# Optimization experiments

Measured on AMD Instinct MI355X. Metric: run time of the kernel, lower is better.

The kernel has to match this reference:

```python
import math
import jax, jax.numpy as jnp
import numpy as np

B, S, IN, D, H, F, E, K, L, C = 4, 1024, 768, 512, 8, 2048, 8, 2, 2, 2
DH = D // H
TEMP = 1.0
LBW = 0.01
EPS = 1e-5


def _sinusoidal_pe(seq_len, dim):
    pos = jnp.arange(seq_len, dtype=jnp.float32)[:, None]
    div = jnp.exp(jnp.arange(0, dim, 2, dtype=jnp.float32) * (-math.log(10000.0) / dim))
    sin = jnp.sin(pos * div)  # [S, D/2]
    cos = jnp.cos(pos * div)  # [S, D/2]
    return jnp.stack([sin, cos], axis=-1).reshape(seq_len, dim)  # interleave even=sin, odd=cos


def _layernorm(x, scale, bias):
    mu = jnp.mean(x, axis=-1, keepdims=True)
    var = jnp.var(x, axis=-1, keepdims=True)
    return (x - mu) * jax.lax.rsqrt(var + EPS) * scale + bias


def _attention(x, w, b):
    # w: [4, D, D] (q, k, v, out), b: [4, D]
    bsz, slen, _ = x.shape
    q = (x @ w[0] + b[0]).reshape(bsz, slen, H, DH)
    k = (x @ w[1] + b[1]).reshape(bsz, slen, H, DH)
    v = (x @ w[2] + b[2]).reshape(bsz, slen, H, DH)
    scores = jnp.einsum('bqhd,bkhd->bhqk', q, k) / math.sqrt(DH)
    attn = jax.nn.softmax(scores, axis=-1)
    out = jnp.einsum('bhqk,bkhd->bqhd', attn, v).reshape(bsz, slen, D)
    return out @ w[3] + b[3]


def _moe(x_flat, gate_w, gate_b, w1, b1, w2, b2):
    # x_flat: [T, D]; gate_w: [D, E]; w1: [E, D, F]; w2: [E, F, D]
    T = x_flat.shape[0]
    gate_logits = (x_flat @ gate_w + gate_b) / TEMP
    gate_scores = jax.nn.softmax(gate_logits, axis=-1)  # [T, E]
    top_v, top_i = jax.lax.top_k(gate_scores, K)        # [T, K]
    top_v = top_v / jnp.sum(top_v, axis=-1, keepdims=True)
    # combine weight per (token, expert): sum over k of topv * one_hot(topi)
    oh = jax.nn.one_hot(top_i, E, dtype=x_flat.dtype)   # [T, K, E]
    combine = jnp.einsum('tk,tke->te', top_v, oh)       # [T, E]
    # dense per-expert FFN (reference for the masked gather/scatter loop)
    h = jax.nn.gelu(jnp.einsum('td,edf->etf', x_flat, w1) + b1[:, None, :], approximate=False)
    expert_out = jnp.einsum('etf,efd->etd', h, w2) + b2[:, None, :]  # [E, T, D]
    y = jnp.einsum('te,etd->td', combine, expert_out)
    # load-balance auxiliary loss
    counts = jnp.sum(oh, axis=(0, 1))                   # [E]
    frac = counts / (T * K)
    routing = jnp.mean(gate_scores, axis=0)
    aux = E * jnp.sum(frac * routing)
    return y, aux


def setup_inputs() -> dict:
    key = jax.random.key(0)
    ks = jax.random.split(key, 10)
    rn = lambda k, shape: jax.random.normal(k, shape, jnp.float32) * 0.02
    return {
        'x': jax.random.normal(ks[0], (B, S, IN), jnp.float32),
        'proj_w': rn(ks[1], (IN, D)), 'proj_b': jnp.zeros((D,), jnp.float32),
        'attn_w': rn(ks[2], (L, 4, D, D)), 'attn_b': jnp.zeros((L, 4, D), jnp.float32),
        'ln1_s': jnp.ones((L, D), jnp.float32), 'ln1_b': jnp.zeros((L, D), jnp.float32),
        'gate_w': rn(ks[3], (L, D, E)), 'gate_b': jnp.zeros((L, E), jnp.float32),
        'w1': rn(ks[4], (L, E, D, F)), 'b1': jnp.zeros((L, E, F), jnp.float32),
        'w2': rn(ks[5], (L, E, F, D)), 'b2': jnp.zeros((L, E, D), jnp.float32),
        'ln2_s': jnp.ones((L, D), jnp.float32), 'ln2_b': jnp.zeros((L, D), jnp.float32),
        'cls_w': rn(ks[6], (D, C)), 'cls_b': jnp.zeros((C,), jnp.float32),
    }


def reference(x, proj_w, proj_b, attn_w, attn_b, ln1_s, ln1_b, gate_w, gate_b,
              w1, b1, w2, b2, ln2_s, ln2_b, cls_w, cls_b):
    h = x @ proj_w + proj_b                       # [B, S, D]
    h = h + _sinusoidal_pe(S, D)[None, :, :]
    total_aux = jnp.zeros((), h.dtype)
    for l in range(L):
        attn_out = _attention(h, attn_w[l], attn_b[l])
        h = _layernorm(h + attn_out, ln1_s[l], ln1_b[l])
        ffn_out, aux = _moe(h.reshape(-1, D), gate_w[l], gate_b[l],
                            w1[l], b1[l], w2[l], b2[l])
        total_aux = total_aux + aux
        h = _layernorm(h + ffn_out.reshape(B, S, D), ln2_s[l], ln2_b[l])
    pooled = jnp.mean(h, axis=1)                  # [B, D]
    logits = pooled @ cls_w + cls_b               # [B, C]
    return logits, LBW * total_aux
```

## Files before the change

kernel.cpp:

```cpp
#include <hip/hip_runtime.h>
#include <math.h>

#define B_ 4
#define S_ 1024
#define IN_ 768
#define D_ 512
#define H_ 8
#define F_ 2048
#define E_ 8
#define KTOP_ 2
#define L_ 2
#define C_ 2
#define DH_ 64
#define T_ (B_*S_)
#define EPS_ 1e-5f
#define LBW_ 0.01f
#define QLD_ (3*D_)
#define NBG_ (T_/256)
#define PSPL_ 16

typedef unsigned short u16;
typedef __attribute__((ext_vector_type(8))) unsigned short u16x8;
typedef __attribute__((ext_vector_type(4))) unsigned short u16x4;
typedef __attribute__((ext_vector_type(8))) short short8;
typedef __attribute__((ext_vector_type(4))) float f32x4;

__device__ __forceinline__ u16 f2b(float f) {
  union { float f; unsigned u; } v; v.f = f;
  const unsigned u = v.u;
  return (u16)((u + 0x7FFFu + ((u >> 16) & 1u)) >> 16);
}
__device__ __forceinline__ float b2f(u16 s) {
  union { unsigned u; float f; } v; v.u = ((unsigned)s) << 16;
  return v.f;
}

__device__ __forceinline__ void gl2lds16(const u16* g, u16* l) {
  __builtin_amdgcn_global_load_lds(
      (const __attribute__((address_space(1))) unsigned int*)g,
      (__attribute__((address_space(3))) unsigned int*)l, 16, 0, 0);
}

__global__ __launch_bounds__(256) void castT(
    const float* __restrict__ W, u16* __restrict__ WT, int K, int N)
{
  __shared__ float tile[32][33];
  const size_t mo = (size_t)blockIdx.z * K * N;
  const int n0 = blockIdx.x * 32, k0 = blockIdx.y * 32;
  const int t = threadIdx.x;
  const int kr = t >> 3, nc4 = (t & 7) * 4;
  const float4 v = *(const float4*)(W + mo + (size_t)(k0 + kr) * N + n0 + nc4);
  tile[kr][nc4+0] = v.x; tile[kr][nc4+1] = v.y;
  tile[kr][nc4+2] = v.z; tile[kr][nc4+3] = v.w;
  __syncthreads();
  const int nr = t >> 3, kc4 = (t & 7) * 4;
  u16x4 o;
  #pragma unroll
  for (int i = 0; i < 4; ++i) o[i] = f2b(tile[kc4 + i][nr]);
  *(u16x4*)(WT + mo + (size_t)(n0 + nr) * K + k0 + kc4) = o;
}

__global__ __launch_bounds__(256) void cast_x(
    const float* __restrict__ X, u16* __restrict__ Xb)
{
  const size_t i = ((size_t)blockIdx.x * 256 + threadIdx.x) * 8;
  const float4 a = *(const float4*)(X + i);
  const float4 b = *(const float4*)(X + i + 4);
  u16x8 o;
  o[0]=f2b(a.x); o[1]=f2b(a.y); o[2]=f2b(a.z); o[3]=f2b(a.w);
  o[4]=f2b(b.x); o[5]=f2b(b.y); o[6]=f2b(b.z); o[7]=f2b(b.w);
  *(u16x8*)(Xb + i) = o;
}

template<int BN, int PE, int GELU, int WF32, int WBF16, int GATHER, int MOE>
__global__ __launch_bounds__(256) void gemm_gl(
    const u16* __restrict__ A, const u16* __restrict__ WTb,
    const float* __restrict__ biasb, float* __restrict__ Cf,
    u16* __restrict__ Cb, int N, int K,
    const int* __restrict__ idx_list, const int* __restrict__ offsets,
    const int* __restrict__ counts)
{
  constexpr int BM = 128;
  constexpr int MI = 4;
  constexpr int MJ = BN / 32;
  constexpr int NIB = BN / 32;
  __shared__ __align__(16) u16 Atile[BM][64];
  __shared__ __align__(16) u16 Btile[BN][64];
  __shared__ int rowsrc[MOE ? BM : 1];

  const int tid = threadIdx.x;
  const int row0 = blockIdx.y * BM, col0 = blockIdx.x * BN;

  int cnt = 0, off = 0;
  const u16* WT = WTb;
  const float* bias = biasb;
  if constexpr (MOE) {
    const int e = blockIdx.z;
    cnt = counts[e];
    if (row0 >= cnt) return;
    off = offsets[e];
    WT  = WTb + (size_t)e * K * N;
    bias = biasb + (size_t)e * N;
    if (tid < BM) {
      const int rr = row0 + tid;
      rowsrc[tid] = (rr < cnt) ? (GATHER ? idx_list[off + rr] : (off + rr)) : 0;
    }
    __syncthreads();
  }

  const int w = tid >> 6, lane = tid & 63;
  const int q15 = lane & 15, g = lane >> 4;
  const int lrow8 = lane >> 3;
  const int scol = ((lane & 7) ^ lrow8) * 8;

  const u16* aptr[4];
  #pragma unroll
  for (int t = 0; t < 4; ++t) {
    const int arow = w * 32 + t * 8 + lrow8;
    int grow;
    if constexpr (MOE) grow = rowsrc[arow];
    else               grow = row0 + arow;
    aptr[t] = A + (size_t)grow * K + scol;
  }
  const u16* bptr[NIB];
  #pragma unroll
  for (int t = 0; t < NIB; ++t) {
    const int brow = w * (BN / 4) + t * 8 + lrow8;
    bptr[t] = WT + (size_t)(col0 + brow) * K + scol;
  }

  const int ar0 = (w >> 1) * 64;
  const int bc0 = (w & 1) * (BN / 2);

  f32x4 acc[MI][MJ];
  #pragma unroll
  for (int i = 0; i < MI; ++i)
    #pragma unroll
    for (int j = 0; j < MJ; ++j) acc[i][j] = (f32x4){0.f, 0.f, 0.f, 0.f};

  for (int k0 = 0; k0 < K; k0 += 64) {
    #pragma unroll
    for (int t = 0; t < 4; ++t)
      gl2lds16(aptr[t] + k0, &Atile[w * 32 + t * 8][0]);
    #pragma unroll
    for (int t = 0; t < NIB; ++t)
      gl2lds16(bptr[t] + k0, &Btile[w * (BN / 4) + t * 8][0]);
    asm volatile("s_waitcnt vmcnt(0)" ::: "memory");
    __syncthreads();
    #pragma unroll
    for (int c = 0; c < 2; ++c) {
      const int ps = ((c * 4 + g) ^ (q15 & 7)) * 8;
      short8 af[MI], bfv[MJ];
      #pragma unroll
      for (int i = 0; i < MI; ++i)
        af[i] = *(const short8*)&Atile[ar0 + i * 16 + q15][ps];
      #pragma unroll
      for (int j = 0; j < MJ; ++j)
        bfv[j] = *(const short8*)&Btile[bc0 + j * 16 + q15][ps];
      #pragma unroll
      for (int i = 0; i < MI; ++i)
        #pragma unroll
        for (int j = 0; j < MJ; ++j)
          acc[i][j] = __builtin_amdgcn_mfma_f32_16x16x32_bf16(af[i], bfv[j], acc[i][j], 0, 0, 0);
    }
    __syncthreads();
  }

  #pragma unroll
  for (int i = 0; i < MI; ++i) {
    #pragma unroll
    for (int r = 0; r < 4; ++r) {
      const int lrow = ar0 + i * 16 + g * 4 + r;
      if constexpr (MOE) {
        const int rr = row0 + lrow;
        if (rr >= cnt) continue;
        const size_t gidx = (size_t)off + rr;
        #pragma unroll
        for (int j = 0; j < MJ; ++j) {
          const int c = col0 + bc0 + j * 16 + q15;
          float vv = acc[i][j][r] + bias[c];
          if (GELU) vv = 0.5f * vv * (1.0f + erff(vv * 0.7071067811865475f));
          if (WF32) Cf[gidx * N + c] = vv;
          if (WBF16) Cb[gidx * N + c] = f2b(vv);
        }
      } else {
        const int row = row0 + lrow;
        #pragma unroll
        for (int j = 0; j < MJ; ++j) {
          const int c = col0 + bc0 + j * 16 + q15;
          float vv = acc[i][j][r] + bias[c];
          if (PE) {
            const float kfac = -0.03597789207803197f;
            const float div = expf((float)(c >> 1) * kfac);
            const float ang = (float)(row & (S_ - 1)) * div;
            vv += (c & 1) ? cosf(ang) : sinf(ang);
          }
          if (WF32) Cf[(size_t)row * N + c] = vv;
          if (WBF16) Cb[(size_t)row * N + c] = f2b(vv);
        }
      }
    }
  }
}

__global__ __launch_bounds__(256) void attn_mfma(
    const u16* __restrict__ qkv, u16* __restrict__ og)
{
  __shared__ u16 Kl[32][72];
  __shared__ u16 VTl[64 * 34];
  const int qt = blockIdx.x;
  const int hh = blockIdx.y & 7, b = blockIdx.y >> 3;
  const int tid = threadIdx.x;
  const int w = tid >> 6, lane = tid & 63;
  const int g = lane >> 4, q15 = lane & 15;
  const int skv = tid >> 3, sd8 = (tid & 7) * 8;

  const size_t qrow = (size_t)(b * S_ + qt * 64 + w * 16 + q15) * QLD_ + hh * 64;
  const short8 qf0 = *(const short8*)(qkv + qrow + g * 8);
  const short8 qf1 = *(const short8*)(qkv + qrow + 32 + g * 8);

  f32x4 o0 = {0.f,0.f,0.f,0.f}, o1 = {0.f,0.f,0.f,0.f};
  f32x4 o2 = {0.f,0.f,0.f,0.f}, o3 = {0.f,0.f,0.f,0.f};
  float m = -1e30f, l = 0.f;

  for (int c0 = 0; c0 < S_; c0 += 32) {
    const size_t srow = (size_t)(b * S_ + c0 + skv) * QLD_ + hh * 64 + sd8;
    const u16x8 kv8 = *(const u16x8*)(qkv + srow + D_);
    const u16x8 vv8 = *(const u16x8*)(qkv + srow + 2 * D_);
    *(u16x8*)&Kl[skv][sd8] = kv8;
    #pragma unroll
    for (int j = 0; j < 8; ++j) {
      const int d = sd8 + j;
      const int kvp = skv ^ (((d >> 5) & 1) << 3);
      VTl[d * 34 + kvp] = vv8[j];
    }
    __syncthreads();

    f32x4 st0 = {0.f,0.f,0.f,0.f}, st1 = {0.f,0.f,0.f,0.f};
    {
      const short8 kf00 = *(const short8*)&Kl[q15][g * 8];
      const short8 kf01 = *(const short8*)&Kl[q15][32 + g * 8];
      const short8 kf10 = *(const short8*)&Kl[16 + q15][g * 8];
      const short8 kf11 = *(const short8*)&Kl[16 + q15][32 + g * 8];
      st0 = __builtin_amdgcn_mfma_f32_16x16x32_bf16(kf00, qf0, st0, 0, 0, 0);
      st0 = __builtin_amdgcn_mfma_f32_16x16x32_bf16(kf01, qf1, st0, 0, 0, 0);
      st1 = __builtin_amdgcn_mfma_f32_16x16x32_bf16(kf10, qf0, st1, 0, 0, 0);
      st1 = __builtin_amdgcn_mfma_f32_16x16x32_bf16(kf11, qf1, st1, 0, 0, 0);
    }

    float s0[4], s1[4];
    #pragma unroll
    for (int r = 0; r < 4; ++r) { s0[r] = st0[r] * 0.125f; s1[r] = st1[r] * 0.125f; }
    float cm = s0[0];
    #pragma unroll
    for (int r = 1; r < 4; ++r) cm = fmaxf(cm, s0[r]);
    #pragma unroll
    for (int r = 0; r < 4; ++r) cm = fmaxf(cm, s1[r]);
    cm = fmaxf(cm, __shfl_xor(cm, 16));
    cm = fmaxf(cm, __shfl_xor(cm, 32));
    const float mn = fmaxf(m, cm);
    const float rsc = __expf(m - mn);
    m = mn;
    float p0[4], p1[4];
    float rs = 0.f;
    #pragma unroll
    for (int r = 0; r < 4; ++r) { p0[r] = __expf(s0[r] - mn); rs += p0[r]; }
    #pragma unroll
    for (int r = 0; r < 4; ++r) { p1[r] = __expf(s1[r] - mn); rs += p1[r]; }
    rs += __shfl_xor(rs, 16);
    rs += __shfl_xor(rs, 32);
    l = l * rsc + rs;

    float rq[4];
    #pragma unroll
    for (int r = 0; r < 4; ++r) rq[r] = __shfl(rsc, 4 * g + r);
    #pragma unroll
    for (int r = 0; r < 4; ++r) {
      o0[r] *= rq[r]; o1[r] *= rq[r]; o2[r] *= rq[r]; o3[r] *= rq[r];
    }

    unsigned pk[4];
    #pragma unroll
    for (int r = 0; r < 4; ++r)
      asm("v_cvt_pk_bf16_f32 %0, %1, %2" : "=v"(pk[r]) : "v"(p0[r]), "v"(p1[r]));
    u16x8 pf;
    #pragma unroll
    for (int j = 0; j < 8; ++j) {
      const int src = q15 + 16 * ((j >> 2) + 2 * (g & 1));
      const unsigned pv = (unsigned)__shfl((int)pk[j & 3], src);
      pf[j] = (g >= 2) ? (u16)(pv >> 16) : (u16)(pv & 0xffffu);
    }
    const short8 pfs = *(const short8*)&pf;

    #pragma unroll
    for (int dt = 0; dt < 4; ++dt) {
      const int gsw = g ^ (dt >> 1);
      const u16* vp = &VTl[(dt * 16 + q15) * 34 + 8 * gsw];
      union { unsigned u[4]; short8 s8; } yv;
      yv.u[0] = *(const unsigned*)(vp + 0);
      yv.u[1] = *(const unsigned*)(vp + 2);
      yv.u[2] = *(const unsigned*)(vp + 4);
      yv.u[3] = *(const unsigned*)(vp + 6);
      if (dt == 0) o0 = __builtin_amdgcn_mfma_f32_16x16x32_bf16(pfs, yv.s8, o0, 0, 0, 0);
      if (dt == 1) o1 = __builtin_amdgcn_mfma_f32_16x16x32_bf16(pfs, yv.s8, o1, 0, 0, 0);
      if (dt == 2) o2 = __builtin_amdgcn_mfma_f32_16x16x32_bf16(pfs, yv.s8, o2, 0, 0, 0);
      if (dt == 3) o3 = __builtin_amdgcn_mfma_f32_16x16x32_bf16(pfs, yv.s8, o3, 0, 0, 0);
    }
    __syncthreads();
  }

  const float linv = 1.0f / l;
  float lq[4];
  #pragma unroll
  for (int r = 0; r < 4; ++r) lq[r] = __shfl(linv, 4 * g + r);
  #pragma unroll
  for (int r = 0; r < 4; ++r) {
    const size_t tok = (size_t)(b * S_ + qt * 64 + w * 16 + 4 * g + r);
    u16* orow = og + tok * D_ + hh * 64 + q15;
    orow[0]  = f2b(o0[r] * lq[r]);
    orow[16] = f2b(o1[r] * lq[r]);
    orow[32] = f2b(o2[r] * lq[r]);
    orow[48] = f2b(o3[r] * lq[r]);
  }
}

__device__ __forceinline__ void load8(const float* p, float* a) {
  const float4 v0 = *(const float4*)p;
  const float4 v1 = *(const float4*)(p + 4);
  a[0]=v0.x; a[1]=v0.y; a[2]=v0.z; a[3]=v0.w;
  a[4]=v1.x; a[5]=v1.y; a[6]=v1.z; a[7]=v1.w;
}

template<int MODE>
__global__ __launch_bounds__(64) void ln_kernel(
    float* __restrict__ h, u16* __restrict__ hb,
    const float* __restrict__ add,
    const float* __restrict__ ebuf, const int* __restrict__ pos_tk,
    const float* __restrict__ topw,
    const float* __restrict__ sc, const float* __restrict__ bi)
{
  const int t = blockIdx.x;
  const int lane = threadIdx.x;
  const int d0 = lane * 8;
  float* hrow = h + (size_t)t * D_;
  float x[8];
  load8(hrow + d0, x);
  if (MODE == 0) {
    float a[8]; load8(add + (size_t)t * D_ + d0, a);
    #pragma unroll
    for (int i = 0; i < 8; ++i) x[i] += a[i];
  } else {
    const float w0 = topw[2*t], w1 = topw[2*t+1];
    const int p0 = pos_tk[2*t], p1 = pos_tk[2*t+1];
    float a[8], b[8];
    load8(ebuf + (size_t)p0 * D_ + d0, a);
    load8(ebuf + (size_t)p1 * D_ + d0, b);
    #pragma unroll
    for (int i = 0; i < 8; ++i) x[i] += w0 * a[i] + w1 * b[i];
  }
  float s = 0.f, ss = 0.f;
  #pragma unroll
  for (int i = 0; i < 8; ++i) { s += x[i]; ss += x[i] * x[i]; }
  #pragma unroll
  for (int off = 32; off > 0; off >>= 1) {
    s  += __shfl_xor(s,  off);
    ss += __shfl_xor(ss, off);
  }
  const float mu = s * (1.f / D_);
  const float var = ss * (1.f / D_) - mu * mu;
  const float rstd = rsqrtf(var + EPS_);
  float g[8], be[8];
  load8(sc + d0, g); load8(bi + d0, be);
  float y[8];
  #pragma unroll
  for (int i = 0; i < 8; ++i) y[i] = (x[i] - mu) * rstd * g[i] + be[i];
  float4 oo0, oo1;
  oo0.x=y[0]; oo0.y=y[1]; oo0.z=y[2]; oo0.w=y[3];
  oo1.x=y[4]; oo1.y=y[5]; oo1.z=y[6]; oo1.w=y[7];
  *(float4*)(hrow + d0) = oo0;
  *(float4*)(hrow + d0 + 4) = oo1;
  u16x8 ob;
  #pragma unroll
  for (int i = 0; i < 8; ++i) ob[i] = f2b(y[i]);
  *(u16x8*)(hb + (size_t)t * D_ + d0) = ob;
}

__global__ __launch_bounds__(256) void gate_kernel(
    const float* __restrict__ h, const float* __restrict__ gw,
    const float* __restrict__ gb,
    int* __restrict__ top_i, float* __restrict__ top_w,
    int* __restrict__ counts_p, float* __restrict__ routing_p)
{
  __shared__ float s_rout[E_];
  __shared__ int s_cnt[E_];
  const int tid = threadIdx.x;
  if (tid < E_) { s_rout[tid] = 0.f; s_cnt[tid] = 0; }
  __syncthreads();
  const int t = blockIdx.x * 256 + tid;
  const float* xr = h + (size_t)t * D_;
  float logit[E_] = {};
  for (int d = 0; d < D_; d += 4) {
    const float4 xv = *(const float4*)(xr + d);
    const float xs[4] = {xv.x, xv.y, xv.z, xv.w};
    #pragma unroll
    for (int i = 0; i < 4; ++i)
      #pragma unroll
      for (int e = 0; e < E_; ++e)
        logit[e] = fmaf(xs[i], gw[(size_t)(d+i) * E_ + e], logit[e]);
  }
  float mx = -1e30f;
  #pragma unroll
  for (int e = 0; e < E_; ++e) { logit[e] += gb[e]; mx = fmaxf(mx, logit[e]); }
  float p[E_]; float sum = 0.f;
  #pragma unroll
  for (int e = 0; e < E_; ++e) { p[e] = expf(logit[e] - mx); sum += p[e]; }
  const float inv = 1.0f / sum;
  #pragma unroll
  for (int e = 0; e < E_; ++e) p[e] *= inv;
  int i0 = 0; float v0 = p[0];
  #pragma unroll
  for (int e = 1; e < E_; ++e) if (p[e] > v0) { v0 = p[e]; i0 = e; }
  int i1 = -1; float v1 = -1.f;
  #pragma unroll
  for (int e = 0; e < E_; ++e) if (e != i0 && p[e] > v1) { v1 = p[e]; i1 = e; }
  const float sw = 1.0f / (v0 + v1);
  top_i[2*t] = i0; top_i[2*t+1] = i1;
  top_w[2*t] = v0 * sw; top_w[2*t+1] = v1 * sw;
  atomicAdd(&s_cnt[i0], 1); atomicAdd(&s_cnt[i1], 1);
  #pragma unroll
  for (int e = 0; e < E_; ++e) atomicAdd(&s_rout[e], p[e]);
  __syncthreads();
  if (tid < E_) {
    counts_p[blockIdx.x * E_ + tid] = s_cnt[tid];
    routing_p[blockIdx.x * E_ + tid] = s_rout[tid];
  }
}

__global__ void gate_scan(
    const int* __restrict__ counts_p, const float* __restrict__ routing_p,
    int* __restrict__ counts, int* __restrict__ offsets,
    int* __restrict__ blk_base, float* __restrict__ aux_acc, int first)
{
  if (threadIdx.x == 0) {
    int cnt[E_]; float rout[E_];
    for (int e = 0; e < E_; ++e) { cnt[e] = 0; rout[e] = 0.f; }
    for (int b = 0; b < NBG_; ++b)
      for (int e = 0; e < E_; ++e) {
        cnt[e] += counts_p[b * E_ + e];
        rout[e] += routing_p[b * E_ + e];
      }
    int off = 0; float aux = 0.f;
    int run[E_];
    for (int e = 0; e < E_; ++e) {
      counts[e] = cnt[e];
      offsets[e] = off; run[e] = off; off += cnt[e];
      aux += ((float)cnt[e] / (float)(T_ * KTOP_)) * (rout[e] / (float)T_);
    }
    for (int b = 0; b < NBG_; ++b)
      for (int e = 0; e < E_; ++e) {
        blk_base[b * E_ + e] = run[e];
        run[e] += counts_p[b * E_ + e];
      }
    const float v = (float)E_ * aux;
    *aux_acc = first ? v : (*aux_acc + v);
  }
}

__global__ __launch_bounds__(256) void gate_fill(
    const int* __restrict__ top_i, const int* __restrict__ blk_base,
    int* __restrict__ idx_list, int* __restrict__ pos_tk)
{
  __shared__ int s_cur[E_];
  const int tid = threadIdx.x;
  if (tid < E_) s_cur[tid] = 0;
  __syncthreads();
  const int t = blockIdx.x * 256 + tid;
  const int e0 = top_i[2*t], e1 = top_i[2*t+1];
  const int r0 = atomicAdd(&s_cur[e0], 1);
  const int r1 = atomicAdd(&s_cur[e1], 1);
  const int g0 = blk_base[blockIdx.x * E_ + e0] + r0;
  const int g1 = blk_base[blockIdx.x * E_ + e1] + r1;
  idx_list[g0] = t; pos_tk[2*t]   = g0;
  idx_list[g1] = t; pos_tk[2*t+1] = g1;
}

__global__ __launch_bounds__(256) void pool_part(
    const float* __restrict__ h, float* __restrict__ ppart)
{
  const int b = blockIdx.y, d0 = blockIdx.x * 64, z = blockIdx.z;
  const int tid = threadIdx.x;
  const int dl = tid & 63, sg = tid >> 6;
  const int s0 = z * (S_ / PSPL_);
  float s = 0.f;
  #pragma unroll
  for (int si = sg; si < S_ / PSPL_; si += 4)
    s += h[((size_t)b * S_ + s0 + si) * D_ + d0 + dl];
  __shared__ float part[4][64];
  part[sg][dl] = s;
  __syncthreads();
  if (tid < 64) {
    const float v = part[0][tid] + part[1][tid] + part[2][tid] + part[3][tid];
    ppart[((size_t)z * B_ + b) * D_ + d0 + tid] = v;
  }
}

__global__ __launch_bounds__(256) void pool_reduce(
    const float* __restrict__ ppart, float* __restrict__ pooled)
{
  const int idx = blockIdx.x * 256 + threadIdx.x;
  float s = 0.f;
  #pragma unroll
  for (int z = 0; z < PSPL_; ++z)
    s += ppart[(size_t)z * B_ * D_ + idx];
  pooled[idx] = s * (1.0f / S_);
}

__global__ __launch_bounds__(64) void cls_kernel(
    const float* __restrict__ pooled, const float* __restrict__ cls_w,
    const float* __restrict__ cls_b, const float* __restrict__ aux_acc,
    float* __restrict__ out)
{
  const int t = threadIdx.x;
  if (t < B_ * C_) {
    const int b = t >> 1, c = t & 1;
    float acc = cls_b[c];
    for (int d = 0; d < D_; ++d)
      acc = fmaf(pooled[b * D_ + d], cls_w[(size_t)d * C_ + c], acc);
    out[b * C_ + c] = acc;
  }
  if (t == 32) out[B_ * C_] = LBW_ * (*aux_acc);
}

extern "C" void kernel_launch(void* const* d_in, const int* in_sizes, int n_in,
                              void* d_out, int out_size, void* d_ws, size_t ws_size,
                              hipStream_t stream) {
  const float* x      = (const float*)d_in[0];
  const float* proj_w = (const float*)d_in[1];
  const float* proj_b = (const float*)d_in[2];
  const float* attn_w = (const float*)d_in[3];
  const float* attn_b = (const float*)d_in[4];
  const float* ln1_s  = (const float*)d_in[5];
  const float* ln1_b  = (const float*)d_in[6];
  const float* gate_w = (const float*)d_in[7];
  const float* gate_b = (const float*)d_in[8];
  const float* w1     = (const float*)d_in[9];
  const float* b1     = (const float*)d_in[10];
  const float* w2     = (const float*)d_in[11];
  const float* b2     = (const float*)d_in[12];
  const float* ln2_s  = (const float*)d_in[13];
  const float* ln2_b  = (const float*)d_in[14];
  const float* cls_w  = (const float*)d_in[15];
  const float* cls_b  = (const float*)d_in[16];
  float* out = (float*)d_out;

  char* base = (char*)d_ws;
  float* h      = (float*)base;                 base += (size_t)T_ * D_ * 4;
  float* t2     = (float*)base;                 base += (size_t)T_ * D_ * 4;
  float* ebuf   = (float*)base;                 base += (size_t)T_ * KTOP_ * D_ * 4;
  u16*   qkvb   = (u16*)base;                   base += (size_t)T_ * QLD_ * 2;
  u16*   x_bf   = (u16*)base;                   base += (size_t)T_ * IN_ * 2;
  u16*   h_bf   = (u16*)base;                   base += (size_t)T_ * D_ * 2;
  u16*   t1_bf  = (u16*)base;                   base += (size_t)T_ * D_ * 2;
  char*  big    = base;                         base += (size_t)T_ * KTOP_ * F_ * 2;
  u16*   wscr   = (u16*)base;                   base += (size_t)E_ * D_ * F_ * 2;
  float* topw   = (float*)base;                 base += (size_t)T_ * KTOP_ * 4;
  int*   counts_p = (int*)base;                 base += NBG_ * E_ * 4;
  float* routing_p= (float*)base;               base += NBG_ * E_ * 4;
  int*   blk_base = (int*)base;                 base += NBG_ * E_ * 4;
  int*   counts = (int*)base;                   base += E_ * 4;
  float* aux_acc= (float*)base;                 base += 4;
  int*   offsets= (int*)base;                   base += E_ * 4;
  int*   top_i  = (int*)base;                   base += (size_t)T_ * KTOP_ * 4;
  int*   idx_list=(int*)base;                   base += (size_t)T_ * KTOP_ * 4;
  int*   pos_tk = (int*)base;                   base += (size_t)T_ * KTOP_ * 4;
  float* pooled = (float*)base;                 base += (size_t)B_ * D_ * 4;
  float* ppart  = (float*)base;                 base += (size_t)PSPL_ * B_ * D_ * 4;

  u16* hbuf_bf = (u16*)big;

  cast_x<<<(T_ * IN_) / 2048, 256, 0, stream>>>(x, x_bf);
  castT<<<dim3(D_/32, IN_/32, 1), 256, 0, stream>>>(proj_w, wscr, IN_, D_);
  gemm_gl<64, 1, 0, 1, 1, 0, 0><<<dim3(D_/64, T_/128), 256, 0, stream>>>(
      x_bf, wscr, proj_b, h, h_bf, D_, IN_, nullptr, nullptr, nullptr);

  for (int l = 0; l < L_; ++l) {
    castT<<<dim3(D_/32, D_/32, 4), 256, 0, stream>>>(
        attn_w + (size_t)l*4*D_*D_, wscr, D_, D_);

    gemm_gl<128, 0, 0, 0, 1, 0, 0><<<dim3(QLD_/128, T_/128), 256, 0, stream>>>(
        h_bf, wscr, attn_b + (size_t)l*4*D_, nullptr, qkvb, QLD_, D_,
        nullptr, nullptr, nullptr);
    attn_mfma<<<dim3(S_/64, B_*H_), 256, 0, stream>>>(qkvb, t1_bf);
    gemm_gl<64, 0, 0, 1, 0, 0, 0><<<dim3(D_/64, T_/128), 256, 0, stream>>>(
        t1_bf, wscr + (size_t)3*D_*D_, attn_b + (size_t)(l*4+3)*D_, t2, nullptr,
        D_, D_, nullptr, nullptr, nullptr);
    ln_kernel<0><<<T_, 64, 0, stream>>>(h, h_bf, t2, nullptr, nullptr, nullptr,
                                        ln1_s + (size_t)l*D_, ln1_b + (size_t)l*D_);

    gate_kernel<<<NBG_, 256, 0, stream>>>(h, gate_w + (size_t)l*D_*E_,
                                          gate_b + (size_t)l*E_,
                                          top_i, topw, counts_p, routing_p);
    gate_scan<<<1, 64, 0, stream>>>(counts_p, routing_p, counts, offsets,
                                    blk_base, aux_acc, l == 0 ? 1 : 0);
    gate_fill<<<NBG_, 256, 0, stream>>>(top_i, blk_base, idx_list, pos_tk);

    castT<<<dim3(F_/32, D_/32, E_), 256, 0, stream>>>(
        w1 + (size_t)l*E_*D_*F_, wscr, D_, F_);
    gemm_gl<128, 0, 1, 0, 1, 1, 1><<<dim3(F_/128, (T_*KTOP_)/128, E_), 256, 0, stream>>>(
        h_bf, wscr, b1 + (size_t)l*E_*F_, nullptr, hbuf_bf,
        F_, D_, idx_list, offsets, counts);
    castT<<<dim3(D_/32, F_/32, E_), 256, 0, stream>>>(
        w2 + (size_t)l*E_*F_*D_, wscr, F_, D_);
    gemm_gl<128, 0, 0, 1, 0, 0, 1><<<dim3(D_/128, (T_*KTOP_)/128, E_), 256, 0, stream>>>(
        hbuf_bf, wscr, b2 + (size_t)l*E_*D_, ebuf, nullptr,
        D_, F_, idx_list, offsets, counts);
    ln_kernel<1><<<T_, 64, 0, stream>>>(h, h_bf, nullptr, ebuf, pos_tk, topw,
                                        ln2_s + (size_t)l*D_, ln2_b + (size_t)l*D_);
  }

  pool_part<<<dim3(D_/64, B_, PSPL_), 256, 0, stream>>>(h, ppart);
  pool_reduce<<<(B_*D_)/256, 256, 0, stream>>>(ppart, pooled);
  cls_kernel<<<1, 64, 0, stream>>>(pooled, cls_w, cls_b, aux_acc, out);
}
```

Measured before the change: 573.7 us.

## Double-buffer LDS tiles in GEMM to overlap global loads with MFMA

Turns the single-stage GEMM main loop into a two-stage LDS ping-pong. The next K-tile is loaded while the current one is consumed, with partial vmcnt waits and raw s_barrier calls. It also raises wave priority with s_setprio around the MFMA section. The goal is to hide global-to-LDS latency, at the cost of doubling LDS use, which may lower occupancy, and of relying on exact vmcnt counts per BN.

```diff
diff --git a/kernel.cpp b/kernel.cpp
--- a/kernel.cpp
+++ b/kernel.cpp
@@ -84,8 +84,8 @@
   constexpr int MI = 4;
   constexpr int MJ = BN / 32;
   constexpr int NIB = BN / 32;
-  __shared__ __align__(16) u16 Atile[BM][64];
-  __shared__ __align__(16) u16 Btile[BN][64];
+  __shared__ __align__(16) u16 Atile[2][BM][64];
+  __shared__ __align__(16) u16 Btile[2][BN][64];
   __shared__ int rowsrc[MOE ? BM : 1];
 
   const int tid = threadIdx.x;
@@ -138,32 +138,48 @@
     #pragma unroll
     for (int j = 0; j < MJ; ++j) acc[i][j] = (f32x4){0.f, 0.f, 0.f, 0.f};
 
-  for (int k0 = 0; k0 < K; k0 += 64) {
+  auto STAGE = [&](int buf, int k0) {
     #pragma unroll
     for (int t = 0; t < 4; ++t)
-      gl2lds16(aptr[t] + k0, &Atile[w * 32 + t * 8][0]);
+      gl2lds16(aptr[t] + k0, &Atile[buf][w * 32 + t * 8][0]);
     #pragma unroll
     for (int t = 0; t < NIB; ++t)
-      gl2lds16(bptr[t] + k0, &Btile[w * (BN / 4) + t * 8][0]);
-    asm volatile("s_waitcnt vmcnt(0)" ::: "memory");
-    __syncthreads();
+      gl2lds16(bptr[t] + k0, &Btile[buf][w * (BN / 4) + t * 8][0]);
+  };
+
+  STAGE(0, 0);
+  const int NT = K >> 6;
+  for (int t = 0; t < NT; ++t) {
+    const int cur = t & 1;
+    if (t + 1 < NT) {
+      STAGE(cur ^ 1, (t + 1) << 6);
+      if constexpr (BN == 128)
+        asm volatile("s_waitcnt vmcnt(8)" ::: "memory");
+      else
+        asm volatile("s_waitcnt vmcnt(6)" ::: "memory");
+    } else {
+      asm volatile("s_waitcnt vmcnt(0)" ::: "memory");
+    }
+    __builtin_amdgcn_s_barrier();
+    __builtin_amdgcn_s_setprio(1);
     #pragma unroll
     for (int c = 0; c < 2; ++c) {
       const int ps = ((c * 4 + g) ^ (q15 & 7)) * 8;
       short8 af[MI], bfv[MJ];
       #pragma unroll
       for (int i = 0; i < MI; ++i)
-        af[i] = *(const short8*)&Atile[ar0 + i * 16 + q15][ps];
+        af[i] = *(const short8*)&Atile[cur][ar0 + i * 16 + q15][ps];
       #pragma unroll
       for (int j = 0; j < MJ; ++j)
-        bfv[j] = *(const short8*)&Btile[bc0 + j * 16 + q15][ps];
+        bfv[j] = *(const short8*)&Btile[cur][bc0 + j * 16 + q15][ps];
       #pragma unroll
       for (int i = 0; i < MI; ++i)
         #pragma unroll
         for (int j = 0; j < MJ; ++j)
           acc[i][j] = __builtin_amdgcn_mfma_f32_16x16x32_bf16(af[i], bfv[j], acc[i][j], 0, 0, 0);
     }
-    __syncthreads();
+    __builtin_amdgcn_s_setprio(0);
+    __builtin_amdgcn_s_barrier();
   }
 
   #pragma unroll
```

New measurement: 583.7 us. Within noise of the previous version (+1.7%).

## Split K across two blocks for out-projection and MoE down GEMMs

Applied to the files above, without the earlier changes.

Adds a KSPLIT template parameter so the attention out-projection and the MoE second GEMM launch twice as many blocks, each covering half the K range. Each half writes its partial sums to a separate slab of doubled fp32 buffers, and the following layernorm kernels add the two partials. The aim is more blocks in flight on these low-occupancy GEMMs. The cost is extra fp32 partial writes and reads in the layernorm kernels, plus a larger workspace.

```diff
diff --git a/kernel.cpp b/kernel.cpp
--- a/kernel.cpp
+++ b/kernel.cpp
@@ -72,7 +72,8 @@
   *(u16x8*)(Xb + i) = o;
 }
 
-template<int BN, int PE, int GELU, int WF32, int WBF16, int GATHER, int MOE>
+template<int BN, int PE, int GELU, int WF32, int WBF16, int GATHER, int MOE,
+         int KSPLIT>
 __global__ __launch_bounds__(256) void gemm_gl(
     const u16* __restrict__ A, const u16* __restrict__ WTb,
     const float* __restrict__ biasb, float* __restrict__ Cf,
@@ -84,6 +85,7 @@
   constexpr int MI = 4;
   constexpr int MJ = BN / 32;
   constexpr int NIB = BN / 32;
+  constexpr int SROWS = MOE ? (T_ * KTOP_) : T_;
   __shared__ __align__(16) u16 Atile[BM][64];
   __shared__ __align__(16) u16 Btile[BN][64];
   __shared__ int rowsrc[MOE ? BM : 1];
@@ -91,11 +93,14 @@
   const int tid = threadIdx.x;
   const int row0 = blockIdx.y * BM, col0 = blockIdx.x * BN;
 
+  int ks = 0;
   int cnt = 0, off = 0;
   const u16* WT = WTb;
   const float* bias = biasb;
   if constexpr (MOE) {
-    const int e = blockIdx.z;
+    int e;
+    if constexpr (KSPLIT == 2) { e = blockIdx.z >> 1; ks = blockIdx.z & 1; }
+    else                       { e = blockIdx.z; }
     cnt = counts[e];
     if (row0 >= cnt) return;
     off = offsets[e];
@@ -106,7 +111,11 @@
       rowsrc[tid] = (rr < cnt) ? (GATHER ? idx_list[off + rr] : (off + rr)) : 0;
     }
     __syncthreads();
-  }
+  } else {
+    if constexpr (KSPLIT == 2) ks = blockIdx.z;
+  }
+  const int k_beg = ks * (K / KSPLIT);
+  const int k_end = k_beg + (K / KSPLIT);
 
   const int w = tid >> 6, lane = tid & 63;
   const int q15 = lane & 15, g = lane >> 4;
@@ -138,7 +147,7 @@
     #pragma unroll
     for (int j = 0; j < MJ; ++j) acc[i][j] = (f32x4){0.f, 0.f, 0.f, 0.f};
 
-  for (int k0 = 0; k0 < K; k0 += 64) {
+  for (int k0 = k_beg; k0 < k_end; k0 += 64) {
     #pragma unroll
     for (int t = 0; t < 4; ++t)
       gl2lds16(aptr[t] + k0, &Atile[w * 32 + t * 8][0]);
@@ -166,6 +175,7 @@
     __syncthreads();
   }
 
+  const size_t srow_off = (size_t)ks * SROWS;
   #pragma unroll
   for (int i = 0; i < MI; ++i) {
     #pragma unroll
@@ -174,29 +184,33 @@
       if constexpr (MOE) {
         const int rr = row0 + lrow;
         if (rr >= cnt) continue;
-        const size_t gidx = (size_t)off + rr;
+        const size_t gidx = (size_t)off + rr + srow_off;
         #pragma unroll
         for (int j = 0; j < MJ; ++j) {
           const int c = col0 + bc0 + j * 16 + q15;
-          float vv = acc[i][j][r] + bias[c];
+          float bv = bias[c];
+          if (KSPLIT == 2 && ks == 1) bv = 0.f;
+          float vv = acc[i][j][r] + bv;
           if (GELU) vv = 0.5f * vv * (1.0f + erff(vv * 0.7071067811865475f));
           if (WF32) Cf[gidx * N + c] = vv;
           if (WBF16) Cb[gidx * N + c] = f2b(vv);
         }
       } else {
-        const int row = row0 + lrow;
+        const size_t row = (size_t)(row0 + lrow) + srow_off;
         #pragma unroll
         for (int j = 0; j < MJ; ++j) {
           const int c = col0 + bc0 + j * 16 + q15;
-          float vv = acc[i][j][r] + bias[c];
+          float bv = bias[c];
+          if (KSPLIT == 2 && ks == 1) bv = 0.f;
+          float vv = acc[i][j][r] + bv;
           if (PE) {
             const float kfac = -0.03597789207803197f;
             const float div = expf((float)(c >> 1) * kfac);
-            const float ang = (float)(row & (S_ - 1)) * div;
+            const float ang = (float)((row0 + lrow) & (S_ - 1)) * div;
             vv += (c & 1) ? cosf(ang) : sinf(ang);
           }
-          if (WF32) Cf[(size_t)row * N + c] = vv;
-          if (WBF16) Cb[(size_t)row * N + c] = f2b(vv);
+          if (WF32) Cf[row * N + c] = vv;
+          if (WBF16) Cb[row * N + c] = f2b(vv);
         }
       }
     }
@@ -346,17 +360,22 @@
   float x[8];
   load8(hrow + d0, x);
   if (MODE == 0) {
-    float a[8]; load8(add + (size_t)t * D_ + d0, a);
-    #pragma unroll
-    for (int i = 0; i < 8; ++i) x[i] += a[i];
+    float a[8], a2[8];
+    load8(add + (size_t)t * D_ + d0, a);
+    load8(add + ((size_t)T_ + t) * D_ + d0, a2);
+    #pragma unroll
+    for (int i = 0; i < 8; ++i) x[i] += a[i] + a2[i];
   } else {
     const float w0 = topw[2*t], w1 = topw[2*t+1];
     const int p0 = pos_tk[2*t], p1 = pos_tk[2*t+1];
-    float a[8], b[8];
+    const size_t SK = (size_t)T_ * KTOP_;
+    float a[8], ab[8], b[8], bb[8];
     load8(ebuf + (size_t)p0 * D_ + d0, a);
+    load8(ebuf + ((size_t)p0 + SK) * D_ + d0, ab);
     load8(ebuf + (size_t)p1 * D_ + d0, b);
-    #pragma unroll
-    for (int i = 0; i < 8; ++i) x[i] += w0 * a[i] + w1 * b[i];
+    load8(ebuf + ((size_t)p1 + SK) * D_ + d0, bb);
+    #pragma unroll
+    for (int i = 0; i < 8; ++i) x[i] += w0 * (a[i] + ab[i]) + w1 * (b[i] + bb[i]);
   }
   float s = 0.f, ss = 0.f;
   #pragma unroll
@@ -555,8 +574,8 @@
 
   char* base = (char*)d_ws;
   float* h      = (float*)base;                 base += (size_t)T_ * D_ * 4;
-  float* t2     = (float*)base;                 base += (size_t)T_ * D_ * 4;
-  float* ebuf   = (float*)base;                 base += (size_t)T_ * KTOP_ * D_ * 4;
+  float* t2     = (float*)base;                 base += (size_t)2 * T_ * D_ * 4;
+  float* ebuf   = (float*)base;                 base += (size_t)2 * T_ * KTOP_ * D_ * 4;
   u16*   qkvb   = (u16*)base;                   base += (size_t)T_ * QLD_ * 2;
   u16*   x_bf   = (u16*)base;                   base += (size_t)T_ * IN_ * 2;
   u16*   h_bf   = (u16*)base;                   base += (size_t)T_ * D_ * 2;
@@ -580,18 +599,18 @@
 
   cast_x<<<(T_ * IN_) / 2048, 256, 0, stream>>>(x, x_bf);
   castT<<<dim3(D_/32, IN_/32, 1), 256, 0, stream>>>(proj_w, wscr, IN_, D_);
-  gemm_gl<64, 1, 0, 1, 1, 0, 0><<<dim3(D_/64, T_/128), 256, 0, stream>>>(
+  gemm_gl<64, 1, 0, 1, 1, 0, 0, 1><<<dim3(D_/64, T_/128), 256, 0, stream>>>(
       x_bf, wscr, proj_b, h, h_bf, D_, IN_, nullptr, nullptr, nullptr);
 
   for (int l = 0; l < L_; ++l) {
     castT<<<dim3(D_/32, D_/32, 4), 256, 0, stream>>>(
         attn_w + (size_t)l*4*D_*D_, wscr, D_, D_);
 
-    gemm_gl<128, 0, 0, 0, 1, 0, 0><<<dim3(QLD_/128, T_/128), 256, 0, stream>>>(
+    gemm_gl<128, 0, 0, 0, 1, 0, 0, 1><<<dim3(QLD_/128, T_/128), 256, 0, stream>>>(
         h_bf, wscr, attn_b + (size_t)l*4*D_, nullptr, qkvb, QLD_, D_,
         nullptr, nullptr, nullptr);
     attn_mfma<<<dim3(S_/64, B_*H_), 256, 0, stream>>>(qkvb, t1_bf);
-    gemm_gl<64, 0, 0, 1, 0, 0, 0><<<dim3(D_/64, T_/128), 256, 0, stream>>>(
+    gemm_gl<64, 0, 0, 1, 0, 0, 0, 2><<<dim3(D_/64, T_/128, 2), 256, 0, stream>>>(
         t1_bf, wscr + (size_t)3*D_*D_, attn_b + (size_t)(l*4+3)*D_, t2, nullptr,
         D_, D_, nullptr, nullptr, nullptr);
     ln_kernel<0><<<T_, 64, 0, stream>>>(h, h_bf, t2, nullptr, nullptr, nullptr,
@@ -606,12 +625,12 @@
 
     castT<<<dim3(F_/32, D_/32, E_), 256, 0, stream>>>(
         w1 + (size_t)l*E_*D_*F_, wscr, D_, F_);
-    gemm_gl<128, 0, 1, 0, 1, 1, 1><<<dim3(F_/128, (T_*KTOP_)/128, E_), 256, 0, stream>>>(
+    gemm_gl<128, 0, 1, 0, 1, 1, 1, 1><<<dim3(F_/128, (T_*KTOP_)/128, E_), 256, 0, stream>>>(
         h_bf, wscr, b1 + (size_t)l*E_*F_, nullptr, hbuf_bf,
         F_, D_, idx_list, offsets, counts);
     castT<<<dim3(D_/32, F_/32, E_), 256, 0, stream>>>(
         w2 + (size_t)l*E_*F_*D_, wscr, F_, D_);
-    gemm_gl<128, 0, 0, 1, 0, 0, 1><<<dim3(D_/128, (T_*KTOP_)/128, E_), 256, 0, stream>>>(
+    gemm_gl<128, 0, 0, 1, 0, 0, 1, 2><<<dim3(D_/128, (T_*KTOP_)/128, 2*E_), 256, 0, stream>>>(
         hbuf_bf, wscr, b2 + (size_t)l*E_*D_, ebuf, nullptr,
         D_, F_, idx_list, offsets, counts);
     ln_kernel<1><<<T_, 64, 0, stream>>>(h, h_bf, nullptr, ebuf, pos_tk, topw,
```

Result: no change. 562.5 us, median of 2 (-1.9%).
